# Performance work log

Measured on AMD Instinct MI355X. Metric: run time of the kernel, lower is better.

## Reference

```python
import jax, jax.numpy as jnp
import numpy as np

B, T_IN, IN = 512, 64, 16
HS, OUT = 32, 32          # Seq2Seq hidden_size; decoder output_size == hidden_size
H = HS * 30               # actual GRU state width = 960
T_PRED = 48


def _p(key, shape, scale=0.05):
    return jax.random.normal(key, shape, dtype=jnp.float32) * scale


def setup_inputs() -> dict:
    key = jax.random.key(0)
    ks = jax.random.split(key, 24)
    G = 3 * H
    return {
        "in_data": jax.random.normal(ks[0], (B, T_IN, IN), dtype=jnp.float32),
        "last_location": jax.random.normal(ks[1], (B, 1, HS), dtype=jnp.float32),
        "pred_length": T_PRED,
        # encoder GRU (2 layers)
        "enc_Wih0": _p(ks[2], (G, IN)), "enc_Whh0": _p(ks[3], (G, H)),
        "enc_bih0": _p(ks[4], (G,)), "enc_bhh0": _p(ks[5], (G,)),
        "enc_Wih1": _p(ks[6], (G, H)), "enc_Whh1": _p(ks[7], (G, H)),
        "enc_bih1": _p(ks[8], (G,)), "enc_bhh1": _p(ks[9], (G,)),
        # decoder GRU (2 layers), input size = HS
        "dec_Wih0": _p(ks[10], (G, HS)), "dec_Whh0": _p(ks[11], (G, H)),
        "dec_bih0": _p(ks[12], (G,)), "dec_bhh0": _p(ks[13], (G,)),
        "dec_Wih1": _p(ks[14], (G, H)), "dec_Whh1": _p(ks[15], (G, H)),
        "dec_bih1": _p(ks[16], (G,)), "dec_bhh1": _p(ks[17], (G,)),
        # output projection H -> OUT
        "lin_W": _p(ks[18], (OUT, H)), "lin_b": _p(ks[19], (OUT,)),
    }


def gru_cell(x, h, Wih, Whh, bih, bhh):
    # PyTorch GRU cell convention (gate order: r, z, n)
    gi = x @ Wih.T + bih
    gh = h @ Whh.T + bhh
    ir, iz, inn = jnp.split(gi, 3, axis=-1)
    hr, hz, hn = jnp.split(gh, 3, axis=-1)
    r = jax.nn.sigmoid(ir + hr)
    z = jax.nn.sigmoid(iz + hz)
    n = jnp.tanh(inn + r * hn)
    return (1.0 - z) * n + z * h


def gru_layer(xs, Wih, Whh, bih, bhh):
    # xs: [T, B, in] time-major; zero initial state
    h0 = jnp.zeros((xs.shape[1], Whh.shape[1]), xs.dtype)
    def step(h, x):
        h2 = gru_cell(x, h, Wih, Whh, bih, bhh)
        return h2, h2
    hT, ys = jax.lax.scan(step, h0, xs)
    return ys, hT


def reference(in_data, last_location, pred_length,
              enc_Wih0, enc_Whh0, enc_bih0, enc_bhh0,
              enc_Wih1, enc_Whh1, enc_bih1, enc_bhh1,
              dec_Wih0, dec_Whh0, dec_bih0, dec_bhh0,
              dec_Wih1, dec_Whh1, dec_bih1, dec_bhh1,
              lin_W, lin_b):
    # ---- encoder: 2-layer GRU over in_data ----
    xs = jnp.transpose(in_data, (1, 0, 2))          # [T, B, IN]
    ys0, h0 = gru_layer(xs, enc_Wih0, enc_Whh0, enc_bih0, enc_bhh0)
    ys1, h1 = gru_layer(ys0, enc_Wih1, enc_Whh1, enc_bih1, enc_bhh1)

    x0 = last_location[:, 0, :]                      # [B, HS]

    def dec_step(carry, _):
        hl0, hl1, x = carry
        hl0 = gru_cell(x, hl0, dec_Wih0, dec_Whh0, dec_bih0, dec_bhh0)
        hl1 = gru_cell(hl0, hl1, dec_Wih1, dec_Whh1, dec_bih1, dec_bhh1)
        # dropout is identity in eval mode
        out = hl1 @ lin_W.T + lin_b                  # [B, OUT]
        hcat = jnp.concatenate([hl0, hl1], axis=-1)  # [B, 2H] (layer-major, as permute+view)
        return (hl0, hl1, out), (out, hcat)

    (_, _, _), (outs, hcats) = jax.lax.scan(dec_step, (h0, h1, x0), None, length=pred_length)
    outputs = jnp.transpose(outs, (1, 0, 2))         # [B, T_pred, OUT]
    hidden_outputs = jnp.transpose(hcats, (1, 0, 2)) # [B, T_pred, 2H]
    return outputs, hidden_outputs
```

## Files before the change

kernel.cpp:

```cpp
#include <hip/hip_runtime.h>
#include <cstdint>
#include <cstddef>

typedef __bf16 bf16;
typedef __bf16 bf16x8 __attribute__((ext_vector_type(8)));
typedef float f32x4 __attribute__((ext_vector_type(4)));

static __device__ __forceinline__ f32x4 mfma16(bf16x8 a, bf16x8 b, f32x4 c) {
  return __builtin_amdgcn_mfma_f32_16x16x32_bf16(a, b, c, 0, 0, 0);
}

struct StepArgs {
  const bf16* X;
  const bf16* Hb;
  const bf16* Wt;
  const float* bA;
  const float* bB;
  const float* Hf_prev;
  float* Hf_next;
  bf16* Hb_next;
  float* out_hidden;
  int ldx;
  int KXPAD;
  int Ktot;
  int _pad;
};

__global__ __launch_bounds__(256) void gru_step(StepArgs a0, StepArgs a1) {
  const StepArgs a = (blockIdx.z == 0) ? a0 : a1;
  const int id = blockIdx.x;
  const int gq = id >> 6, bm = (id >> 3) & 7, gr = id & 7;
  const int g = gq * 8 + gr;
  if (g >= 30) return;

  __shared__ bf16 ldsB[4 * 3840];

  const int tid = threadIdx.x;
  const int wv = tid >> 6, lane = tid & 63, col = lane & 15, quad = lane >> 4;
  const int mh = wv & 1, uh = wv >> 1;
  const int Ktot = a.Ktot, KXPAD = a.KXPAD;
  const int nb = tid >> 3, cc = tid & 7;

  const bf16* Wb0 = a.Wt + ((size_t)g * 96 + nb) * Ktot + cc * 4;
  const size_t WrS = (size_t)32 * Ktot;
  char* ldsW = (char*)ldsB + nb * 80 + cc * 8;

  const int rowA = bm * 64 + mh * 32 + col;
  const bf16* Xrow = a.X + (size_t)rowA * a.ldx + quad * 8;
  const bf16* Hrow = a.Hb + (size_t)rowA * 960 + quad * 8 - KXPAD;
  const int ldx16 = 16 * a.ldx;

  const int uu = uh * 16 + col;
  const int u = g * 32 + uu;
  const int gbase = g * 96;
  const float bAr = a.bA[gbase + uu];
  const float bAz = a.bA[gbase + 32 + uu];
  const float bAn = a.bA[gbase + 64 + uu];
  const float bBn = a.bB[gbase + 64 + uu];
  const int mb0 = bm * 64 + mh * 32 + quad * 4;
  float hold[2][4];
#pragma unroll
  for (int mf = 0; mf < 2; ++mf)
#pragma unroll
    for (int r = 0; r < 4; ++r)
      hold[mf][r] = a.Hf_prev[(size_t)(mb0 + mf * 16 + r) * 960 + u];

  const f32x4 z4 = {0.f, 0.f, 0.f, 0.f};
  f32x4 acc[2][3] = {{z4, z4, z4}, {z4, z4, z4}};
  f32x4 ck0 = z4, ck1 = z4;

  uint2 br0[6], br1[6];
  bf16x8 ar0[4], ar1[4];

#define STAGEP(PH, K) do { int _ka = (K); int _kb = _ka + 32; if (_kb >= Ktot) _kb = 0; \
    br##PH[0] = *(const uint2*)(Wb0 + _ka); \
    br##PH[1] = *(const uint2*)(Wb0 + WrS + _ka); \
    br##PH[2] = *(const uint2*)(Wb0 + 2 * WrS + _ka); \
    br##PH[3] = *(const uint2*)(Wb0 + _kb); \
    br##PH[4] = *(const uint2*)(Wb0 + WrS + _kb); \
    br##PH[5] = *(const uint2*)(Wb0 + 2 * WrS + _kb); } while (0)

#define LOADA1(D0, D1, KK) do { int _k1 = (KK); \
    if (_k1 < KXPAD) { const bf16* _p = Xrow + _k1; D0 = *(const bf16x8*)_p; D1 = *(const bf16x8*)(_p + ldx16); } \
    else { const bf16* _p = Hrow + _k1; D0 = *(const bf16x8*)_p; D1 = *(const bf16x8*)(_p + 16 * 960); } } while (0)

#define LOADAP(PH, K) do { int _ka2 = (K); int _kb2 = _ka2 + 32; if (_kb2 >= Ktot) _kb2 = 0; \
    LOADA1(ar##PH[0], ar##PH[1], _ka2); LOADA1(ar##PH[2], ar##PH[3], _kb2); } while (0)

  const char* ldsRd = (char*)ldsB + (uh * 16 + col) * 80 + quad * 16;

#define BARRIER() do { \
    asm volatile("s_waitcnt lgkmcnt(0)" ::: "memory"); \
    __builtin_amdgcn_s_barrier(); \
    asm volatile("" ::: "memory"); } while (0)

#define GRU_PAIR(PH) do { \
    if (k0 == KXPAD) { ck0 = acc[0][2]; ck1 = acc[1][2]; } \
    char* _d = ldsW + bufoff; \
    *(uint2*)(_d)               = br##PH[0]; \
    *(uint2*)(_d + 2560)        = br##PH[1]; \
    *(uint2*)(_d + 5120)        = br##PH[2]; \
    *(uint2*)(_d + 7680)        = br##PH[3]; \
    *(uint2*)(_d + 7680 + 2560) = br##PH[4]; \
    *(uint2*)(_d + 7680 + 5120) = br##PH[5]; \
    bf16x8 am0 = ar##PH[0], am1 = ar##PH[1], am2 = ar##PH[2], am3 = ar##PH[3]; \
    BARRIER(); \
    { int _k2 = k0 + 128; if (_k2 >= Ktot) _k2 = 0; STAGEP(PH, _k2); LOADAP(PH, _k2); } \
    const char* _rp = ldsRd + bufoff; \
    _Pragma("unroll") \
    for (int gate = 0; gate < 3; ++gate) { \
      bf16x8 _bf = *(const bf16x8*)(_rp + gate * 2560); \
      acc[0][gate] = mfma16(am0, _bf, acc[0][gate]); \
      acc[1][gate] = mfma16(am1, _bf, acc[1][gate]); \
    } \
    if (k0 + 32 == KXPAD) { ck0 = acc[0][2]; ck1 = acc[1][2]; } \
    _Pragma("unroll") \
    for (int gate = 0; gate < 3; ++gate) { \
      bf16x8 _bf = *(const bf16x8*)(_rp + 7680 + gate * 2560); \
      acc[0][gate] = mfma16(am2, _bf, acc[0][gate]); \
      acc[1][gate] = mfma16(am3, _bf, acc[1][gate]); \
    } \
    k0 += 64; bufoff ^= 15360; \
  } while (0)

#define TAILT(PH) do { \
    char* _d = ldsW + bufoff; \
    *(uint2*)(_d)        = br##PH[0]; \
    *(uint2*)(_d + 2560) = br##PH[1]; \
    *(uint2*)(_d + 5120) = br##PH[2]; \
    bf16x8 am0 = ar##PH[0], am1 = ar##PH[1]; \
    BARRIER(); \
    const char* _rp = ldsRd + bufoff; \
    _Pragma("unroll") \
    for (int gate = 0; gate < 3; ++gate) { \
      bf16x8 _bf = *(const bf16x8*)(_rp + gate * 2560); \
      acc[0][gate] = mfma16(am0, _bf, acc[0][gate]); \
      acc[1][gate] = mfma16(am1, _bf, acc[1][gate]); \
    } \
  } while (0)

  STAGEP(0, 0);
  STAGEP(1, 64);
  LOADAP(0, 0);
  LOADAP(1, 64);
  int k0 = 0, bufoff = 0;
  const int T32 = Ktot >> 5;
  const int npair = T32 >> 1;
  for (int it = 0; it + 2 <= npair; it += 2) {
    GRU_PAIR(0);
    GRU_PAIR(1);
  }
  if (npair & 1) { GRU_PAIR(0); }
  if (T32 & 1) {
    if (k0 == KXPAD) { ck0 = acc[0][2]; ck1 = acc[1][2]; }
    if (npair & 1) TAILT(1); else TAILT(0);
  }

#undef GRU_PAIR
#undef TAILT
#undef BARRIER
#undef STAGEP
#undef LOADAP
#undef LOADA1

#pragma unroll
  for (int mf = 0; mf < 2; ++mf) {
    f32x4 R = acc[mf][0], Z = acc[mf][1], Nf = acc[mf][2];
    f32x4 Nx = mf ? ck1 : ck0;
    const int mbase = mb0 + mf * 16;
#pragma unroll
    for (int r = 0; r < 4; ++r) {
      const int mm = mbase + r;
      float rg = 1.f / (1.f + __expf(-(R[r] + bAr)));
      float zg = 1.f / (1.f + __expf(-(Z[r] + bAz)));
      float inn = Nx[r] + bAn;
      float hn = (Nf[r] - Nx[r]) + bBn;
      float ng = tanhf(fmaf(rg, hn, inn));
      float hnew = fmaf(zg, hold[mf][r] - ng, ng);
      a.Hf_next[(size_t)mm * 960 + u] = hnew;
      a.Hb_next[(size_t)mm * 960 + u] = (bf16)hnew;
      if (a.out_hidden) a.out_hidden[(size_t)mm * 92160 + u] = hnew;
    }
  }
}

__global__ __launch_bounds__(256) void final_linear(const float* __restrict__ hid,
                                                    const bf16* __restrict__ Wb,
                                                    const float* __restrict__ bias,
                                                    float* __restrict__ outp) {
  const int tid = threadIdx.x;
  const int wv = tid >> 6, lane = tid & 63, col = lane & 15, quad = lane >> 4;
  const int row = blockIdx.x * 64 + wv * 16 + col;
  const int b = row / 48, t = row - b * 48;
  const float* arow = hid + (size_t)b * 92160 + (size_t)t * 1920 + 960 + quad * 8;
  const f32x4 z4 = {0.f, 0.f, 0.f, 0.f};
  f32x4 acc0 = z4, acc1 = z4;
  for (int k0 = 0; k0 < 960; k0 += 32) {
    f32x4 x0 = *(const f32x4*)(arow + k0);
    f32x4 x1 = *(const f32x4*)(arow + k0 + 4);
    bf16x8 af;
#pragma unroll
    for (int i = 0; i < 4; ++i) { af[i] = (bf16)x0[i]; af[4 + i] = (bf16)x1[i]; }
    bf16x8 b0 = *(const bf16x8*)(Wb + (size_t)col * 960 + k0 + quad * 8);
    bf16x8 b1 = *(const bf16x8*)(Wb + (size_t)(16 + col) * 960 + k0 + quad * 8);
    acc0 = mfma16(af, b0, acc0);
    acc1 = mfma16(af, b1, acc1);
  }
  const int mbase = blockIdx.x * 64 + wv * 16 + quad * 4;
#pragma unroll
  for (int r = 0; r < 4; ++r) {
    const int mm = mbase + r;
    const int b2 = mm / 48, t2 = mm - b2 * 48;
    float* o = outp + (size_t)b2 * 1536 + (size_t)t2 * 32;
    o[col] = acc0[r] + bias[col];
    o[16 + col] = acc1[r] + bias[16 + col];
  }
}

__global__ void prep_weight(const float* __restrict__ Wih, const float* __restrict__ Whh,
                            bf16* __restrict__ dst, int Kx, int KXPAD, int Ktot) {
  const int total = 2880 * Ktot;
  for (int e = blockIdx.x * blockDim.x + threadIdx.x; e < total; e += gridDim.x * blockDim.x) {
    int n = e / Ktot, k = e - n * Ktot;
    int g = n / 96, loc = n - g * 96, gate = loc >> 5, uu = loc & 31;
    int c = gate * 960 + g * 32 + uu;
    float v;
    if (k < KXPAD) v = (k < Kx) ? Wih[(size_t)c * Kx + k] : 0.f;
    else v = Whh[(size_t)c * 960 + (k - KXPAD)];
    dst[e] = (bf16)v;
  }
}

__global__ void prep_weight_dec0(const float* __restrict__ Wih, const float* __restrict__ Whh,
                                 const float* __restrict__ linW, bf16* __restrict__ dst) {
  const int total = 2880 * 1920;
  for (int e = blockIdx.x * blockDim.x + threadIdx.x; e < total; e += gridDim.x * blockDim.x) {
    int n = e / 1920, k = e - n * 1920;
    int g = n / 96, loc = n - g * 96, gate = loc >> 5, uu = loc & 31;
    int c = gate * 960 + g * 32 + uu;
    float v;
    if (k < 960) {
      float s = 0.f;
      for (int j = 0; j < 32; ++j) s = fmaf(Wih[(size_t)c * 32 + j], linW[(size_t)j * 960 + k], s);
      v = s;
    } else {
      v = Whh[(size_t)c * 960 + (k - 960)];
    }
    dst[e] = (bf16)v;
  }
}

__global__ void prep_bias(const float* __restrict__ bih, const float* __restrict__ bhh,
                          float* __restrict__ bA, float* __restrict__ bB) {
  int n = blockIdx.x * blockDim.x + threadIdx.x;
  if (n >= 2880) return;
  int g = n / 96, loc = n - g * 96, gate = loc >> 5, uu = loc & 31;
  int c = gate * 960 + g * 32 + uu;
  if (gate < 2) { bA[n] = bih[c] + bhh[c]; bB[n] = 0.f; }
  else          { bA[n] = bih[c];          bB[n] = bhh[c]; }
}

__global__ void prep_bias_dec0(const float* __restrict__ bih, const float* __restrict__ bhh,
                               const float* __restrict__ Wih, const float* __restrict__ linb,
                               float* __restrict__ bA, float* __restrict__ bB) {
  int n = blockIdx.x * blockDim.x + threadIdx.x;
  if (n >= 2880) return;
  int g = n / 96, loc = n - g * 96, gate = loc >> 5, uu = loc & 31;
  int c = gate * 960 + g * 32 + uu;
  float bi = bih[c];
  for (int j = 0; j < 32; ++j) bi = fmaf(Wih[(size_t)c * 32 + j], linb[j], bi);
  if (gate < 2) { bA[n] = bi + bhh[c]; bB[n] = 0.f; }
  else          { bA[n] = bi;          bB[n] = bhh[c]; }
}

__global__ void prep_xenc(const float* __restrict__ in_data, bf16* __restrict__ X) {
  int i = blockIdx.x * blockDim.x + threadIdx.x;
  if (i >= 64 * 512 * 32) return;
  int k = i & 31, m = (i >> 5) & 511, t = i >> 14;
  X[i] = (k < 16) ? (bf16)in_data[((size_t)m * 64 + t) * 16 + k] : (bf16)0.f;
}

__global__ void cvt_bf16(const float* __restrict__ s, bf16* __restrict__ d, int n) {
  int i = blockIdx.x * blockDim.x + threadIdx.x;
  if (i < n) d[i] = (bf16)s[i];
}

extern "C" void kernel_launch(void* const* d_in, const int* in_sizes, int n_in,
                              void* d_out, int out_size, void* d_ws, size_t ws_size,
                              hipStream_t stream) {
  (void)in_sizes; (void)n_in; (void)out_size; (void)ws_size;
  const float* in_data = (const float*)d_in[0];
  const float* last_loc = (const float*)d_in[1];
  const float* eWih0 = (const float*)d_in[3];
  const float* eWhh0 = (const float*)d_in[4];
  const float* ebih0 = (const float*)d_in[5];
  const float* ebhh0 = (const float*)d_in[6];
  const float* eWih1 = (const float*)d_in[7];
  const float* eWhh1 = (const float*)d_in[8];
  const float* ebih1 = (const float*)d_in[9];
  const float* ebhh1 = (const float*)d_in[10];
  const float* dWih0 = (const float*)d_in[11];
  const float* dWhh0 = (const float*)d_in[12];
  const float* dbih0 = (const float*)d_in[13];
  const float* dbhh0 = (const float*)d_in[14];
  const float* dWih1 = (const float*)d_in[15];
  const float* dWhh1 = (const float*)d_in[16];
  const float* dbih1 = (const float*)d_in[17];
  const float* dbhh1 = (const float*)d_in[18];
  const float* linW = (const float*)d_in[19];
  const float* linb = (const float*)d_in[20];
  float* outp = (float*)d_out;

  uint8_t* base = (uint8_t*)d_ws;
  size_t off = 0;
  auto alloc = [&](size_t bytes) -> void* {
    void* p = base + off;
    off += (bytes + 255) & ~(size_t)255;
    return p;
  };
  bf16* WtE0 = (bf16*)alloc(2880ull * 992 * 2);
  bf16* WtE1 = (bf16*)alloc(2880ull * 1920 * 2);
  bf16* WtD0a = (bf16*)alloc(2880ull * 992 * 2);
  bf16* WtD0 = (bf16*)alloc(2880ull * 1920 * 2);
  bf16* WtD1 = (bf16*)alloc(2880ull * 1920 * 2);
  bf16* linWb = (bf16*)alloc(32ull * 960 * 2);
  float* bA_e0 = (float*)alloc(2880 * 4); float* bB_e0 = (float*)alloc(2880 * 4);
  float* bA_e1 = (float*)alloc(2880 * 4); float* bB_e1 = (float*)alloc(2880 * 4);
  float* bA_d0a = (float*)alloc(2880 * 4); float* bB_d0a = (float*)alloc(2880 * 4);
  float* bA_d0 = (float*)alloc(2880 * 4); float* bB_d0 = (float*)alloc(2880 * 4);
  float* bA_d1 = (float*)alloc(2880 * 4); float* bB_d1 = (float*)alloc(2880 * 4);
  bf16* Xenc = (bf16*)alloc(64ull * 512 * 32 * 2);
  bf16* Xloc = (bf16*)alloc(512ull * 32 * 2);
  const int HS_ELEMS = 512 * 960;
  float* states = (float*)alloc((size_t)HS_ELEMS * (4 * 4 + 4 * 2));
  float* h0f[2] = {states, states + HS_ELEMS};
  float* h1f[2] = {states + 2 * HS_ELEMS, states + 3 * HS_ELEMS};
  bf16* bstates = (bf16*)(states + 4 * HS_ELEMS);
  bf16* h0b[2] = {bstates, bstates + HS_ELEMS};
  bf16* h1b[2] = {bstates + 2 * HS_ELEMS, bstates + 3 * HS_ELEMS};

  hipMemsetAsync(states, 0, (size_t)HS_ELEMS * (4 * 4 + 4 * 2), stream);
  prep_weight<<<4096, 256, 0, stream>>>(eWih0, eWhh0, WtE0, 16, 32, 992);
  prep_weight<<<8192, 256, 0, stream>>>(eWih1, eWhh1, WtE1, 960, 960, 1920);
  prep_weight<<<4096, 256, 0, stream>>>(dWih0, dWhh0, WtD0a, 32, 32, 992);
  prep_weight_dec0<<<8192, 256, 0, stream>>>(dWih0, dWhh0, linW, WtD0);
  prep_weight<<<8192, 256, 0, stream>>>(dWih1, dWhh1, WtD1, 960, 960, 1920);
  prep_bias<<<12, 256, 0, stream>>>(ebih0, ebhh0, bA_e0, bB_e0);
  prep_bias<<<12, 256, 0, stream>>>(ebih1, ebhh1, bA_e1, bB_e1);
  prep_bias<<<12, 256, 0, stream>>>(dbih0, dbhh0, bA_d0a, bB_d0a);
  prep_bias_dec0<<<12, 256, 0, stream>>>(dbih0, dbhh0, dWih0, linb, bA_d0, bB_d0);
  prep_bias<<<12, 256, 0, stream>>>(dbih1, dbhh1, bA_d1, bB_d1);
  prep_xenc<<<(64 * 512 * 32 + 255) / 256, 256, 0, stream>>>(in_data, Xenc);
  cvt_bf16<<<(512 * 32 + 255) / 256, 256, 0, stream>>>(last_loc, Xloc, 512 * 32);
  cvt_bf16<<<(32 * 960 + 255) / 256, 256, 0, stream>>>(linW, linWb, 32 * 960);

  auto step_args = [](const bf16* X, int ldx, const bf16* Hb, const bf16* Wt,
                      const float* bA, const float* bB, int KXPAD, int Ktot,
                      const float* Hfp, float* Hfn, bf16* Hbn, float* oh) {
    StepArgs s;
    s.X = X; s.ldx = ldx; s.Hb = Hb; s.Wt = Wt; s.bA = bA; s.bB = bB;
    s.KXPAD = KXPAD; s.Ktot = Ktot; s.Hf_prev = Hfp; s.Hf_next = Hfn;
    s.Hb_next = Hbn; s.out_hidden = oh; s._pad = 0;
    return s;
  };

  int p0 = 0, p1 = 0;
  {
    StepArgs s = step_args(Xenc, 32, h0b[p0], WtE0, bA_e0, bB_e0, 32, 992,
                           h0f[p0], h0f[1 - p0], h0b[1 - p0], nullptr);
    gru_step<<<dim3(256, 1, 1), 256, 0, stream>>>(s, s);
    p0 ^= 1;
  }
  for (int t = 1; t < 64; ++t) {
    StepArgs s0 = step_args(Xenc + (size_t)t * 512 * 32, 32, h0b[p0], WtE0, bA_e0, bB_e0, 32, 992,
                            h0f[p0], h0f[1 - p0], h0b[1 - p0], nullptr);
    StepArgs s1 = step_args(h0b[p0], 960, h1b[p1], WtE1, bA_e1, bB_e1, 960, 1920,
                            h1f[p1], h1f[1 - p1], h1b[1 - p1], nullptr);
    gru_step<<<dim3(256, 1, 2), 256, 0, stream>>>(s0, s1);
    p0 ^= 1; p1 ^= 1;
  }
  {
    StepArgs s1 = step_args(h0b[p0], 960, h1b[p1], WtE1, bA_e1, bB_e1, 960, 1920,
                            h1f[p1], h1f[1 - p1], h1b[1 - p1], nullptr);
    gru_step<<<dim3(256, 1, 1), 256, 0, stream>>>(s1, s1);
    p1 ^= 1;
  }
  float* hid = outp + 786432;
  for (int t = 0; t < 48; ++t) {
    StepArgs s0;
    if (t == 0)
      s0 = step_args(Xloc, 32, h0b[p0], WtD0a, bA_d0a, bB_d0a, 32, 992,
                     h0f[p0], h0f[1 - p0], h0b[1 - p0], hid + (size_t)t * 1920);
    else
      s0 = step_args(h1b[p1], 960, h0b[p0], WtD0, bA_d0, bB_d0, 960, 1920,
                     h0f[p0], h0f[1 - p0], h0b[1 - p0], hid + (size_t)t * 1920);
    gru_step<<<dim3(256, 1, 1), 256, 0, stream>>>(s0, s0);
    p0 ^= 1;
    StepArgs s1 = step_args(h0b[p0], 960, h1b[p1], WtD1, bA_d1, bB_d1, 960, 1920,
                            h1f[p1], h1f[1 - p1], h1b[1 - p1], hid + (size_t)t * 1920 + 960);
    gru_step<<<dim3(256, 1, 1), 256, 0, stream>>>(s1, s1);
    p1 ^= 1;
  }
  final_linear<<<384, 256, 0, stream>>>(hid, linWb, linb, outp);
}
```

Measured before the change: 5.018 ms.

## Replace per-step GRU kernel launches with one persistent kernel using grid barriers

Replaces the ~161 separate gru_step launches with a single persistent kernel of 512 blocks that runs every encoder and decoder timestep, separated by software grid barriers built from per-step atomic counters. State loads and stores become relaxed agent-scope atomics so values written by other blocks are visible after each barrier. This removes per-launch overhead and the tail gaps between dependent steps. In exchange it relies on all 512 blocks being co-resident (launch bounds of 2 blocks per CU), adds barrier spin cost, and the atomic loads may be less efficient than plain vector loads.

```diff
diff --git a/kernel.cpp b/kernel.cpp
--- a/kernel.cpp
+++ b/kernel.cpp
@@ -8,6 +8,23 @@
 
 static __device__ __forceinline__ f32x4 mfma16(bf16x8 a, bf16x8 b, f32x4 c) {
   return __builtin_amdgcn_mfma_f32_16x16x32_bf16(a, b, c, 0, 0, 0);
+}
+
+static __device__ __forceinline__ bf16x8 ld_state16(const bf16* p) {
+  union { bf16x8 v; unsigned long long q[2]; } u;
+  u.q[0] = __hip_atomic_load((unsigned long long*)p, __ATOMIC_RELAXED, __HIP_MEMORY_SCOPE_AGENT);
+  u.q[1] = __hip_atomic_load((unsigned long long*)p + 1, __ATOMIC_RELAXED, __HIP_MEMORY_SCOPE_AGENT);
+  return u.v;
+}
+static __device__ __forceinline__ float ld_statef(const float* p) {
+  return __hip_atomic_load((float*)p, __ATOMIC_RELAXED, __HIP_MEMORY_SCOPE_AGENT);
+}
+static __device__ __forceinline__ void st_statef(float* p, float v) {
+  __hip_atomic_store(p, v, __ATOMIC_RELAXED, __HIP_MEMORY_SCOPE_AGENT);
+}
+static __device__ __forceinline__ void st_stateh(bf16* p, float v) {
+  union { bf16 h; unsigned short s; } c; c.h = (bf16)v;
+  __hip_atomic_store((unsigned short*)p, c.s, __ATOMIC_RELAXED, __HIP_MEMORY_SCOPE_AGENT);
 }
 
 struct StepArgs {
@@ -26,14 +43,11 @@
   int _pad;
 };
 
-__global__ __launch_bounds__(256) void gru_step(StepArgs a0, StepArgs a1) {
-  const StepArgs a = (blockIdx.z == 0) ? a0 : a1;
-  const int id = blockIdx.x;
+static __device__ __forceinline__ void gru_step_body(const StepArgs a, int id) {
+  __shared__ bf16 ldsB[4 * 3840];
+
   const int gq = id >> 6, bm = (id >> 3) & 7, gr = id & 7;
   const int g = gq * 8 + gr;
-  if (g >= 30) return;
-
-  __shared__ bf16 ldsB[4 * 3840];
 
   const int tid = threadIdx.x;
   const int wv = tid >> 6, lane = tid & 63, col = lane & 15, quad = lane >> 4;
@@ -63,7 +77,7 @@
   for (int mf = 0; mf < 2; ++mf)
 #pragma unroll
     for (int r = 0; r < 4; ++r)
-      hold[mf][r] = a.Hf_prev[(size_t)(mb0 + mf * 16 + r) * 960 + u];
+      hold[mf][r] = ld_statef(a.Hf_prev + (size_t)(mb0 + mf * 16 + r) * 960 + u);
 
   const f32x4 z4 = {0.f, 0.f, 0.f, 0.f};
   f32x4 acc[2][3] = {{z4, z4, z4}, {z4, z4, z4}};
@@ -81,15 +95,15 @@
     br##PH[5] = *(const uint2*)(Wb0 + 2 * WrS + _kb); } while (0)
 
 #define LOADA1(D0, D1, KK) do { int _k1 = (KK); \
-    if (_k1 < KXPAD) { const bf16* _p = Xrow + _k1; D0 = *(const bf16x8*)_p; D1 = *(const bf16x8*)(_p + ldx16); } \
-    else { const bf16* _p = Hrow + _k1; D0 = *(const bf16x8*)_p; D1 = *(const bf16x8*)(_p + 16 * 960); } } while (0)
+    if (_k1 < KXPAD) { const bf16* _p = Xrow + _k1; D0 = ld_state16(_p); D1 = ld_state16(_p + ldx16); } \
+    else { const bf16* _p = Hrow + _k1; D0 = ld_state16(_p); D1 = ld_state16(_p + 16 * 960); } } while (0)
 
 #define LOADAP(PH, K) do { int _ka2 = (K); int _kb2 = _ka2 + 32; if (_kb2 >= Ktot) _kb2 = 0; \
     LOADA1(ar##PH[0], ar##PH[1], _ka2); LOADA1(ar##PH[2], ar##PH[3], _kb2); } while (0)
 
   const char* ldsRd = (char*)ldsB + (uh * 16 + col) * 80 + quad * 16;
 
-#define BARRIER() do { \
+#define KBARRIER() do { \
     asm volatile("s_waitcnt lgkmcnt(0)" ::: "memory"); \
     __builtin_amdgcn_s_barrier(); \
     asm volatile("" ::: "memory"); } while (0)
@@ -104,7 +118,7 @@
     *(uint2*)(_d + 7680 + 2560) = br##PH[4]; \
     *(uint2*)(_d + 7680 + 5120) = br##PH[5]; \
     bf16x8 am0 = ar##PH[0], am1 = ar##PH[1], am2 = ar##PH[2], am3 = ar##PH[3]; \
-    BARRIER(); \
+    KBARRIER(); \
     { int _k2 = k0 + 128; if (_k2 >= Ktot) _k2 = 0; STAGEP(PH, _k2); LOADAP(PH, _k2); } \
     const char* _rp = ldsRd + bufoff; \
     _Pragma("unroll") \
@@ -129,7 +143,7 @@
     *(uint2*)(_d + 2560) = br##PH[1]; \
     *(uint2*)(_d + 5120) = br##PH[2]; \
     bf16x8 am0 = ar##PH[0], am1 = ar##PH[1]; \
-    BARRIER(); \
+    KBARRIER(); \
     const char* _rp = ldsRd + bufoff; \
     _Pragma("unroll") \
     for (int gate = 0; gate < 3; ++gate) { \
@@ -158,7 +172,7 @@
 
 #undef GRU_PAIR
 #undef TAILT
-#undef BARRIER
+#undef KBARRIER
 #undef STAGEP
 #undef LOADAP
 #undef LOADA1
@@ -177,10 +191,105 @@
       float hn = (Nf[r] - Nx[r]) + bBn;
       float ng = tanhf(fmaf(rg, hn, inn));
       float hnew = fmaf(zg, hold[mf][r] - ng, ng);
-      a.Hf_next[(size_t)mm * 960 + u] = hnew;
-      a.Hb_next[(size_t)mm * 960 + u] = (bf16)hnew;
+      st_statef(a.Hf_next + (size_t)mm * 960 + u, hnew);
+      st_stateh(a.Hb_next + (size_t)mm * 960 + u, hnew);
       if (a.out_hidden) a.out_hidden[(size_t)mm * 92160 + u] = hnew;
     }
+  }
+}
+
+static __device__ __forceinline__ void grid_barrier(unsigned* cnt) {
+  __syncthreads();
+  if (threadIdx.x == 0) {
+    __hip_atomic_fetch_add(cnt + (blockIdx.x >> 5) * 16, 1u, __ATOMIC_RELAXED, __HIP_MEMORY_SCOPE_AGENT);
+  }
+  if (threadIdx.x < 16) {
+    unsigned* myp = cnt + threadIdx.x * 16;
+    while (__hip_atomic_load(myp, __ATOMIC_RELAXED, __HIP_MEMORY_SCOPE_AGENT) < 32u) {
+      __builtin_amdgcn_s_sleep(1);
+    }
+  }
+  __syncthreads();
+  asm volatile("" ::: "memory");
+}
+
+struct PP {
+  const bf16 *Xenc, *Xloc;
+  const bf16 *WtE0, *WtE1, *WtD0a, *WtD0, *WtD1;
+  const float *bAe0, *bBe0, *bAe1, *bBe1, *bAd0a, *bBd0a, *bAd0, *bBd0, *bAd1, *bBd1;
+  float *h0f0, *h0f1, *h1f0, *h1f1;
+  bf16 *h0b0, *h0b1, *h1b0, *h1b1;
+  float *hid;
+  unsigned *bars;
+};
+
+__global__ __launch_bounds__(256, 2) void gru_persistent(PP P) {
+  const int bid = blockIdx.x;
+  const int unit = bid >> 8;
+  const int id = bid & 255;
+  const int g = ((id >> 6) << 3) + (id & 7);
+  const bool alive = (g < 30);
+  int bi = 0;
+
+  auto mkargs = [](const bf16* X, int ldx, const bf16* Hb, const bf16* Wt,
+                   const float* bA, const float* bB, int KXPAD, int Ktot,
+                   const float* Hfp, float* Hfn, bf16* Hbn, float* oh) {
+    StepArgs s;
+    s.X = X; s.ldx = ldx; s.Hb = Hb; s.Wt = Wt; s.bA = bA; s.bB = bB;
+    s.KXPAD = KXPAD; s.Ktot = Ktot; s.Hf_prev = Hfp; s.Hf_next = Hfn;
+    s.Hb_next = Hbn; s.out_hidden = oh; s._pad = 0;
+    return s;
+  };
+
+  for (int p = 0; p <= 64; ++p) {
+    if (alive && unit == 0 && p < 64) {
+      const bf16* hbi = (p & 1) ? P.h0b1 : P.h0b0;
+      const float* hfi = (p & 1) ? P.h0f1 : P.h0f0;
+      float* hfo = (p & 1) ? P.h0f0 : P.h0f1;
+      bf16* hbo = (p & 1) ? P.h0b0 : P.h0b1;
+      StepArgs s = mkargs(P.Xenc + (size_t)p * 512 * 32, 32, hbi, P.WtE0,
+                          P.bAe0, P.bBe0, 32, 992, hfi, hfo, hbo, nullptr);
+      gru_step_body(s, id);
+    } else if (alive && unit == 1 && p >= 1) {
+      const bf16* xs = (p & 1) ? P.h0b1 : P.h0b0;
+      const bf16* hbi = (p & 1) ? P.h1b0 : P.h1b1;
+      const float* hfi = (p & 1) ? P.h1f0 : P.h1f1;
+      float* hfo = (p & 1) ? P.h1f1 : P.h1f0;
+      bf16* hbo = (p & 1) ? P.h1b1 : P.h1b0;
+      StepArgs s = mkargs(xs, 960, hbi, P.WtE1, P.bAe1, P.bBe1, 960, 1920,
+                          hfi, hfo, hbo, nullptr);
+      gru_step_body(s, id);
+    }
+    grid_barrier(P.bars + (size_t)(bi++) * 256);
+  }
+
+  for (int t = 0; t < 48; ++t) {
+    if (alive && unit == 0) {
+      const bf16* hbi = (t & 1) ? P.h0b1 : P.h0b0;
+      const float* hfi = (t & 1) ? P.h0f1 : P.h0f0;
+      float* hfo = (t & 1) ? P.h0f0 : P.h0f1;
+      bf16* hbo = (t & 1) ? P.h0b0 : P.h0b1;
+      StepArgs s;
+      if (t == 0)
+        s = mkargs(P.Xloc, 32, hbi, P.WtD0a, P.bAd0a, P.bBd0a, 32, 992,
+                   hfi, hfo, hbo, P.hid);
+      else
+        s = mkargs((t & 1) ? P.h1b1 : P.h1b0, 960, hbi, P.WtD0, P.bAd0, P.bBd0,
+                   960, 1920, hfi, hfo, hbo, P.hid + (size_t)t * 1920);
+      gru_step_body(s, id);
+    }
+    grid_barrier(P.bars + (size_t)(bi++) * 256);
+    if (alive && unit == 1) {
+      const bf16* xs = (t & 1) ? P.h0b0 : P.h0b1;
+      const bf16* hbi = (t & 1) ? P.h1b1 : P.h1b0;
+      const float* hfi = (t & 1) ? P.h1f1 : P.h1f0;
+      float* hfo = (t & 1) ? P.h1f0 : P.h1f1;
+      bf16* hbo = (t & 1) ? P.h1b0 : P.h1b1;
+      StepArgs s = mkargs(xs, 960, hbi, P.WtD1, P.bAd1, P.bBd1, 960, 1920,
+                          hfi, hfo, hbo, P.hid + (size_t)t * 1920 + 960);
+      gru_step_body(s, id);
+    }
+    grid_barrier(P.bars + (size_t)(bi++) * 256);
   }
 }
 
@@ -333,6 +442,7 @@
   bf16* Xloc = (bf16*)alloc(512ull * 32 * 2);
   const int HS_ELEMS = 512 * 960;
   float* states = (float*)alloc((size_t)HS_ELEMS * (4 * 4 + 4 * 2));
+  unsigned* bars = (unsigned*)alloc(161ull * 1024);
   float* h0f[2] = {states, states + HS_ELEMS};
   float* h1f[2] = {states + 2 * HS_ELEMS, states + 3 * HS_ELEMS};
   bf16* bstates = (bf16*)(states + 4 * HS_ELEMS);
@@ -340,6 +450,7 @@
   bf16* h1b[2] = {bstates + 2 * HS_ELEMS, bstates + 3 * HS_ELEMS};
 
   hipMemsetAsync(states, 0, (size_t)HS_ELEMS * (4 * 4 + 4 * 2), stream);
+  hipMemsetAsync(bars, 0, 161ull * 1024, stream);
   prep_weight<<<4096, 256, 0, stream>>>(eWih0, eWhh0, WtE0, 16, 32, 992);
   prep_weight<<<8192, 256, 0, stream>>>(eWih1, eWhh1, WtE1, 960, 960, 1920);
   prep_weight<<<4096, 256, 0, stream>>>(dWih0, dWhh0, WtD0a, 32, 32, 992);
@@ -354,52 +465,19 @@
   cvt_bf16<<<(512 * 32 + 255) / 256, 256, 0, stream>>>(last_loc, Xloc, 512 * 32);
   cvt_bf16<<<(32 * 960 + 255) / 256, 256, 0, stream>>>(linW, linWb, 32 * 960);
 
-  auto step_args = [](const bf16* X, int ldx, const bf16* Hb, const bf16* Wt,
-                      const float* bA, const float* bB, int KXPAD, int Ktot,
-                      const float* Hfp, float* Hfn, bf16* Hbn, float* oh) {
-    StepArgs s;
-    s.X = X; s.ldx = ldx; s.Hb = Hb; s.Wt = Wt; s.bA = bA; s.bB = bB;
-    s.KXPAD = KXPAD; s.Ktot = Ktot; s.Hf_prev = Hfp; s.Hf_next = Hfn;
-    s.Hb_next = Hbn; s.out_hidden = oh; s._pad = 0;
-    return s;
-  };
-
-  int p0 = 0, p1 = 0;
-  {
-    StepArgs s = step_args(Xenc, 32, h0b[p0], WtE0, bA_e0, bB_e0, 32, 992,
-                           h0f[p0], h0f[1 - p0], h0b[1 - p0], nullptr);
-    gru_step<<<dim3(256, 1, 1), 256, 0, stream>>>(s, s);
-    p0 ^= 1;
-  }
-  for (int t = 1; t < 64; ++t) {
-    StepArgs s0 = step_args(Xenc + (size_t)t * 512 * 32, 32, h0b[p0], WtE0, bA_e0, bB_e0, 32, 992,
-                            h0f[p0], h0f[1 - p0], h0b[1 - p0], nullptr);
-    StepArgs s1 = step_args(h0b[p0], 960, h1b[p1], WtE1, bA_e1, bB_e1, 960, 1920,
-                            h1f[p1], h1f[1 - p1], h1b[1 - p1], nullptr);
-    gru_step<<<dim3(256, 1, 2), 256, 0, stream>>>(s0, s1);
-    p0 ^= 1; p1 ^= 1;
-  }
-  {
-    StepArgs s1 = step_args(h0b[p0], 960, h1b[p1], WtE1, bA_e1, bB_e1, 960, 1920,
-                            h1f[p1], h1f[1 - p1], h1b[1 - p1], nullptr);
-    gru_step<<<dim3(256, 1, 1), 256, 0, stream>>>(s1, s1);
-    p1 ^= 1;
-  }
   float* hid = outp + 786432;
-  for (int t = 0; t < 48; ++t) {
-    StepArgs s0;
-    if (t == 0)
-      s0 = step_args(Xloc, 32, h0b[p0], WtD0a, bA_d0a, bB_d0a, 32, 992,
-                     h0f[p0], h0f[1 - p0], h0b[1 - p0], hid + (size_t)t * 1920);
-    else
-      s0 = step_args(h1b[p1], 960, h0b[p0], WtD0, bA_d0, bB_d0, 960, 1920,
-                     h0f[p0], h0f[1 - p0], h0b[1 - p0], hid + (size_t)t * 1920);
-    gru_step<<<dim3(256, 1, 1), 256, 0, stream>>>(s0, s0);
-    p0 ^= 1;
-    StepArgs s1 = step_args(h0b[p0], 960, h1b[p1], WtD1, bA_d1, bB_d1, 960, 1920,
-                            h1f[p1], h1f[1 - p1], h1b[1 - p1], hid + (size_t)t * 1920 + 960);
-    gru_step<<<dim3(256, 1, 1), 256, 0, stream>>>(s1, s1);
-    p1 ^= 1;
-  }
+
+  PP P;
+  P.Xenc = Xenc; P.Xloc = Xloc;
+  P.WtE0 = WtE0; P.WtE1 = WtE1; P.WtD0a = WtD0a; P.WtD0 = WtD0; P.WtD1 = WtD1;
+  P.bAe0 = bA_e0; P.bBe0 = bB_e0; P.bAe1 = bA_e1; P.bBe1 = bB_e1;
+  P.bAd0a = bA_d0a; P.bBd0a = bB_d0a; P.bAd0 = bA_d0; P.bBd0 = bB_d0;
+  P.bAd1 = bA_d1; P.bBd1 = bB_d1;
+  P.h0f0 = h0f[0]; P.h0f1 = h0f[1]; P.h1f0 = h1f[0]; P.h1f1 = h1f[1];
+  P.h0b0 = h0b[0]; P.h0b1 = h0b[1]; P.h1b0 = h1b[0]; P.h1b1 = h1b[1];
+  P.hid = hid; P.bars = bars;
+
+  gru_persistent<<<dim3(512, 1, 1), 256, 0, stream>>>(P);
+
   final_linear<<<384, 256, 0, stream>>>(hid, linWb, linb, outp);
 }
```

Result: slower. 9.985 ms (+99.0%).
